# Optimization experiments

Measured on AMD Instinct MI355X. Metric: run time of the kernel, lower is better.

## Reference

```python
import jax, jax.numpy as jnp
import numpy as np

LN_EPS = 1e-5


def setup_inputs() -> dict:
    key = jax.random.key(0)
    ks = jax.random.split(key, 6)
    N_NODES, N_EDGES, D, H, E = 100000, 20000, 128, 64, 1000000
    node_feat = jax.random.normal(ks[0], (N_NODES, D), dtype=jnp.float32)
    edge_feat = jax.random.normal(ks[1], (N_EDGES, D), dtype=jnp.float32)
    gamma = jnp.ones((2 * D,), dtype=jnp.float32)
    beta = jnp.zeros((2 * D,), dtype=jnp.float32)
    # xavier_uniform-like init
    lim1 = float(np.sqrt(6.0 / (2 * D + H)))
    lim2 = float(np.sqrt(6.0 / (H + 1)))
    W1 = jax.random.uniform(ks[2], (2 * D, H), minval=-lim1, maxval=lim1, dtype=jnp.float32)
    b1 = jnp.zeros((H,), dtype=jnp.float32)
    W2 = jax.random.uniform(ks[3], (H, 1), minval=-lim2, maxval=lim2, dtype=jnp.float32)
    b2 = jnp.zeros((1,), dtype=jnp.float32)
    node_idx = jax.random.randint(ks[4], (E,), 0, N_NODES, dtype=jnp.int64 if jax.config.read('jax_enable_x64') else jnp.int32)
    edge_idx = jax.random.randint(ks[5], (E,), 0, N_EDGES, dtype=node_idx.dtype)
    return {"node_feat": node_feat, "edge_feat": edge_feat, "gamma": gamma, "beta": beta,
            "W1": W1, "b1": b1, "W2": W2, "b2": b2,
            "node_idx": node_idx, "edge_idx": edge_idx}


def reference(node_feat, edge_feat, gamma, beta, W1, b1, W2, b2, node_idx, edge_idx):
    # Gather incidence-pair embeddings: [E, D] each
    emb_node = node_feat[node_idx]
    emb_edge = edge_feat[edge_idx]
    # combined: [E, 2D], order = [edge, node] as in torch.cat([emb_edge, emb_node], 1)
    combined = jnp.concatenate([emb_edge, emb_node], axis=1)
    # LayerNorm over last dim
    mu = jnp.mean(combined, axis=-1, keepdims=True)
    var = jnp.var(combined, axis=-1, keepdims=True)
    xn = (combined - mu) * jax.lax.rsqrt(var + LN_EPS) * gamma + beta
    # MLP: Linear -> ReLU -> Linear, output [E, 1]
    h = jax.nn.relu(xn @ W1 + b1)
    return h @ W2 + b2
```

## Files before the change

### kernel.cpp

```cpp
#include <hip/hip_runtime.h>

#define LN_EPS 1e-5f
#define DD 128
#define TWO_D 256
#define HH 64
#define PPB 512

typedef unsigned int uint;
typedef unsigned short ushort;
typedef __attribute__((ext_vector_type(8))) short short8v;
typedef __attribute__((ext_vector_type(4))) float f32x4;

__device__ __forceinline__ ushort f2bf(float f) {
    uint u = __float_as_uint(f);
    u += 0x7FFFu + ((u >> 16) & 1u);
    return (ushort)(u >> 16);
}
__device__ __forceinline__ float bf2f(ushort h) {
    return __uint_as_float(((uint)h) << 16);
}
__device__ __forceinline__ int clampi(int v, int lo, int hi) {
    return v < lo ? lo : (v > hi ? hi : v);
}
__device__ __forceinline__ uint lsb8(uint a, uint b) {
    uint nx = (((a & 0x01010101u) * 0x08040201u) >> 24) & 0xFu;
    uint ny = (((b & 0x01010101u) * 0x08040201u) >> 24) & 0xFu;
    return (nx << 4) | ny;
}

__global__ __launch_bounds__(256) void k_fused(
    const float* __restrict__ node_feat, int n_nodes, int nbN,
    const float* __restrict__ edge_feat, int n_edges,
    const float* __restrict__ gamma, const float* __restrict__ beta,
    const float* __restrict__ W1, const float* __restrict__ b1,
    const float* __restrict__ W2,
    signed char* __restrict__ node_pt, signed char* __restrict__ edge_pt,
    float* __restrict__ GB) {
    int bid = blockIdx.x;
    int tid = threadIdx.x;

    if (bid == 0) {
        if (tid < 128) {
            int h = tid & 63;
            bool isB = tid >= 64;
            float acc = isB ? b1[h] : 0.f;
            const float* coef = isB ? beta : gamma;
#pragma unroll 8
            for (int d = 0; d < TWO_D; ++d)
                acc = fmaf(coef[d], W1[d * HH + h], acc);
            GB[tid] = acc;
        }
        __syncthreads();
        if (tid < 64) {
            int h = ((tid & 3) * 16) + (tid >> 2);
            GB[128 + tid] = GB[h];
            GB[192 + tid] = GB[64 + h];
            GB[256 + tid] = W2[h];
        }
        return;
    }

    const float* feat;
    int nrows, gofs, rbase0;
    signed char* pt;
    if (bid <= nbN) {
        feat = node_feat; nrows = n_nodes; gofs = 128;
        rbase0 = (bid - 1) * 128; pt = node_pt;
    } else {
        feat = edge_feat; nrows = n_edges; gofs = 0;
        rbase0 = (bid - 1 - nbN) * 128; pt = edge_pt;
    }

    __shared__ __align__(16) char lds[49664];
    uint* sqLDS = (uint*)(lds + 49152);

    {
        int l = tid & 63;
        int w = tid >> 6;
#pragma unroll
        for (int ci = 0; ci < 4; ++ci) {
            int combo = ci * 4 + w;
            int ks = combo & 3;
            int ht = combo >> 2;
            int kbase = gofs + ks * 32 + (l >> 4) * 8;
            int h = ht * 16 + (l & 15);
            short8v v;
#pragma unroll
            for (int j = 0; j < 8; ++j)
                v[j] = (short)f2bf(gamma[kbase + j] * W1[(size_t)(kbase + j) * HH + h]);
            *(short8v*)(lds + 32768 + combo * 1024 + l * 16) = v;
        }
    }

    {
        float4 tmp[16];
#pragma unroll
        for (int u = 0; u < 16; ++u) {
            int F4 = u * 256 + tid;
            int r = F4 >> 5;
            int rg = rbase0 + r;
            rg = rg < nrows ? rg : (nrows - 1);
            int c4 = (F4 & 31) * 4;
            tmp[u] = *(const float4*)&feat[(size_t)rg * DD + c4];
        }
#pragma unroll
        for (int u = 0; u < 16; ++u) {
            int F4 = u * 256 + tid;
            int r = F4 >> 5;
            int c4 = (F4 & 31) * 4;
            uint2 wv;
            wv.x = (uint)f2bf(tmp[u].x) | ((uint)f2bf(tmp[u].y) << 16);
            wv.y = (uint)f2bf(tmp[u].z) | ((uint)f2bf(tmp[u].w) << 16);
            int byte = (r * 256 + c4 * 2) ^ ((r & 7) << 4);
            *(uint2*)(lds + byte) = wv;
        }
    }

    __syncthreads();

    int w = tid >> 6;
    int lane = tid & 63;
    f32x4 acc[2][4];
#pragma unroll
    for (int i = 0; i < 2; ++i)
#pragma unroll
        for (int j = 0; j < 4; ++j) acc[i][j] = (f32x4){0.f, 0.f, 0.f, 0.f};

    int arow_lo = lane & 15;
    int akofs = (lane >> 4) * 8;
#pragma unroll
    for (int ks = 0; ks < 4; ++ks) {
        int kk = ks * 32 + akofs;
        int rr0 = (2 * w) * 16 + arow_lo;
        int rr1 = rr0 + 16;
        short8v a0 = *(const short8v*)(lds + ((rr0 * 256 + kk * 2) ^ ((rr0 & 7) << 4)));
        short8v a1 = *(const short8v*)(lds + ((rr1 * 256 + kk * 2) ^ ((rr1 & 7) << 4)));
#pragma unroll
        for (int ht = 0; ht < 4; ++ht) {
            short8v b = *(const short8v*)(lds + 32768 + (ht * 4 + ks) * 1024 + lane * 16);
            acc[0][ht] = __builtin_amdgcn_mfma_f32_16x16x32_bf16(a0, b, acc[0][ht], 0, 0, 0);
            acc[1][ht] = __builtin_amdgcn_mfma_f32_16x16x32_bf16(a1, b, acc[1][ht], 0, 0, 0);
        }
    }

    {
        int row = tid >> 1, half = tid & 1;
        float s = 0.f, q = 0.f;
#pragma unroll
        for (int i = 0; i < 8; ++i) {
            int byte = (row * 256 + half * 128 + i * 16) ^ ((row & 7) << 4);
            short8v v = *(const short8v*)(lds + byte);
#pragma unroll
            for (int j = 0; j < 8; ++j) {
                float x = bf2f((ushort)v[j]);
                s += x;
                q = fmaf(x, x, q);
            }
        }
        s += __shfl_xor(s, 1);
        q += __shfl_xor(q, 1);
        if (half == 0) {
            int sq = clampi(__float2int_rn(2.0f * s), -127, 127);
            int qq = clampi(__float2int_rn((q - 128.0f) * (1.0f / 0.75f)), -127, 127);
            sqLDS[row] = ((uint)sq & 0xFFu) | (((uint)qq & 0xFFu) << 8);
        }
    }

    __syncthreads();

    {
        int colh = lane & 15;
        int rquad = lane >> 4;
#pragma unroll
        for (int rt = 0; rt < 2; ++rt)
#pragma unroll
            for (int reg = 0; reg < 4; ++reg) {
                float m = fmaxf(fmaxf(fabsf(acc[rt][0][reg]), fabsf(acc[rt][1][reg])),
                                fmaxf(fabsf(acc[rt][2][reg]), fabsf(acc[rt][3][reg])));
                m = fmaxf(m, __shfl_xor(m, 1));
                m = fmaxf(m, __shfl_xor(m, 2));
                m = fmaxf(m, __shfl_xor(m, 4));
                m = fmaxf(m, __shfl_xor(m, 8));
                m = fmaxf(m, 1e-20f);
                float inv = 127.0f / m;
                int rl = (2 * w + rt) * 16 + rquad * 4 + reg;
                uint P = sqLDS[rl] | ((uint)f2bf(m * (1.0f / 127.0f)) << 16);
                uint pk = 0;
#pragma unroll
                for (int ht = 0; ht < 4; ++ht) {
                    uint byte;
                    if (colh < 8) {
                        int kpos = colh * 4 + ht;
                        uint V = (P >> (8 * (kpos >> 3))) & 0xFFu;
                        uint bit = (V >> (7 - (kpos & 7))) & 1u;
                        int q7 = clampi(__float2int_rn(acc[rt][ht][reg] * inv * 0.5f), -63, 63);
                        byte = (((uint)q7 << 1) | bit) & 0xFFu;
                    } else {
                        byte = (uint)__float2int_rn(acc[rt][ht][reg] * inv) & 0xFFu;
                    }
                    pk |= byte << (8 * ht);
                }
                if (rbase0 + rl < nrows)
                    *(uint*)&pt[(size_t)(rbase0 + rl) * 64 + colh * 4] = pk;
            }
    }
}

__global__ __launch_bounds__(256) void k_pairs(const int* __restrict__ node_idx,
                                               const int* __restrict__ edge_idx,
                                               const signed char* __restrict__ node_pt,
                                               const signed char* __restrict__ edge_pt,
                                               const float* __restrict__ GB,
                                               const float* __restrict__ b2,
                                               float* __restrict__ out, int E) {
    __shared__ int sNi[PPB];
    __shared__ int sEi[PPB];
    int tid = threadIdx.x;
    int base = blockIdx.x * PPB;
    int cnt = E - base;
    cnt = cnt < PPB ? cnt : PPB;
    for (int i = tid; i < cnt; i += 256) {
        sNi[i] = node_idx[base + i];
        sEi[i] = edge_idx[base + i];
    }
    __syncthreads();

    int l = tid & 3;
    int grp = tid >> 2;

    float G16[16], B16[16], W16[16];
#pragma unroll
    for (int j4 = 0; j4 < 4; ++j4) {
        float4 g = *(const float4*)&GB[128 + l * 16 + j4 * 4];
        float4 b = *(const float4*)&GB[192 + l * 16 + j4 * 4];
        float4 wv = *(const float4*)&GB[256 + l * 16 + j4 * 4];
        G16[j4 * 4 + 0] = g.x; G16[j4 * 4 + 1] = g.y; G16[j4 * 4 + 2] = g.z; G16[j4 * 4 + 3] = g.w;
        B16[j4 * 4 + 0] = b.x; B16[j4 * 4 + 1] = b.y; B16[j4 * 4 + 2] = b.z; B16[j4 * 4 + 3] = b.w;
        W16[j4 * 4 + 0] = wv.x; W16[j4 * 4 + 1] = wv.y; W16[j4 * 4 + 2] = wv.z; W16[j4 * 4 + 3] = wv.w;
    }
    float b2v = b2[0];
    int s_l = (l < 2) ? 1 : 0;
    float two_s = (l < 2) ? 2.0f : 1.0f;

    for (int it = 0; it < PPB; it += 256) {
        uint4 qe[4], qn[4];
        int iv[4];
#pragma unroll
        for (int u = 0; u < 4; ++u) {
            int i = it + u * 64 + grp;
            iv[u] = i;
            int ii = i < cnt ? i : 0;
            int ni = sNi[ii];
            int ei = sEi[ii];
            qe[u] = *(const uint4*)&edge_pt[(size_t)ei * 64 + l * 16];
            qn[u] = *(const uint4*)&node_pt[(size_t)ni * 64 + l * 16];
        }
#pragma unroll
        for (int u = 0; u < 4; ++u) {
            uint4 e = qe[u], n = qn[u];
            uint uu = lsb8(e.x, e.y) | (lsb8(e.z, e.w) << 8) |
                      (lsb8(n.x, n.y) << 16) | (lsb8(n.z, n.w) << 24);
            uint t0 = __shfl((int)uu, 0, 4);
            uint t1 = __shfl((int)uu, 1, 4);

            float S = 0.5f * ((float)(int)(signed char)(t0 & 0xFFu) +
                              (float)(int)(signed char)((t0 >> 16) & 0xFFu));
            float Q = 256.0f + 0.75f * ((float)(int)(signed char)((t0 >> 8) & 0xFFu) +
                                        (float)(int)(signed char)(t0 >> 24));
            float esc = bf2f((ushort)(t1 & 0xFFFFu)) * two_s;
            float nsc = bf2f((ushort)(t1 >> 16)) * two_s;

            float mu = S * (1.f / TWO_D);
            float var = fmaf(Q, 1.f / TWO_D, -mu * mu);
            float rstd = rsqrtf(var + LN_EPS);
            float nmu = -mu;

            uint ew[4] = {e.x, e.y, e.z, e.w};
            uint nw[4] = {n.x, n.y, n.z, n.w};
            float acc = 0.f;
#pragma unroll
            for (int j = 0; j < 16; ++j) {
                int sh = (3 - (j & 3)) * 8;
                int qa = ((int)(ew[j >> 2] << sh)) >> (24 + s_l);
                int qb = ((int)(nw[j >> 2] << sh)) >> (24 + s_l);
                float v = fmaf((float)qa, esc, (float)qb * nsc);
                float t = fmaf(nmu, G16[j], v);
                float hv = fmaf(rstd, t, B16[j]);
                hv = fmaxf(hv, 0.f);
                acc = fmaf(hv, W16[j], acc);
            }

            acc += __shfl_xor(acc, 1);
            acc += __shfl_xor(acc, 2);

            if (l == 0 && iv[u] < cnt) out[base + iv[u]] = acc + b2v;
        }
    }
}

extern "C" void kernel_launch(void* const* d_in, const int* in_sizes, int n_in,
                              void* d_out, int out_size, void* d_ws, size_t ws_size,
                              hipStream_t stream) {
    const float* node_feat = (const float*)d_in[0];
    const float* edge_feat = (const float*)d_in[1];
    const float* gamma = (const float*)d_in[2];
    const float* beta = (const float*)d_in[3];
    const float* W1 = (const float*)d_in[4];
    const float* b1 = (const float*)d_in[5];
    const float* W2 = (const float*)d_in[6];
    const float* b2 = (const float*)d_in[7];
    const int* node_idx = (const int*)d_in[8];
    const int* edge_idx = (const int*)d_in[9];

    int n_nodes = in_sizes[0] / DD;
    int n_edges = in_sizes[1] / DD;
    int E = in_sizes[8];

    char* wsb = (char*)d_ws;
    size_t o = 0;
    float* GB = (float*)(wsb + o); o += 2048;
    o = (o + 127) & ~(size_t)127;
    signed char* node_pt = (signed char*)(wsb + o); o += (size_t)n_nodes * 64;
    signed char* edge_pt = (signed char*)(wsb + o); o += (size_t)n_edges * 64;

    int nbN = (n_nodes + 127) / 128;
    int nbE = (n_edges + 127) / 128;

    k_fused<<<1 + nbN + nbE, 256, 0, stream>>>(node_feat, n_nodes, nbN,
                                               edge_feat, n_edges,
                                               gamma, beta, W1, b1, W2,
                                               node_pt, edge_pt, GB);
    k_pairs<<<(E + PPB - 1) / PPB, 256, 0, stream>>>(node_idx, edge_idx, node_pt, edge_pt,
                                                     GB, b2, (float*)d_out, E);
}
```

Measured before the change: 51.02 us.

## Bin incidence pairs by node index range before gathering packed rows

Adds histogram, scan and scatter kernels that sort the pairs into 8 buckets by node index range and pack node and edge indices into one record. A new pairs kernel walks each bucket so the concurrent node-row gathers hit a smaller slice of the packed node table, improving cache locality. The cost is three extra launches plus writing and reading an 8-byte-per-pair binned array, and output writes become scattered.

```diff
diff --git a/kernel.cpp b/kernel.cpp
--- a/kernel.cpp
+++ b/kernel.cpp
@@ -206,6 +206,181 @@
     }
 }
 
+__global__ __launch_bounds__(256) void k_hist(const int* __restrict__ node_idx, int E,
+                                              int chunk, float scale,
+                                              uint* __restrict__ hist) {
+    __shared__ uint lc[8];
+    int tid = threadIdx.x;
+    if (tid < 8) lc[tid] = 0;
+    __syncthreads();
+    int s = blockIdx.x * chunk;
+    int e = s + chunk < E ? s + chunk : E;
+    for (int p = s + tid; p < e; p += 256) {
+        int ni = __builtin_nontemporal_load(&node_idx[p]);
+        int b = (int)((float)ni * scale);
+        b = b < 7 ? b : 7;
+        atomicAdd(&lc[b], 1u);
+    }
+    __syncthreads();
+    if (tid < 8) hist[blockIdx.x * 8 + tid] = lc[tid];
+}
+
+__global__ __launch_bounds__(256) void k_scan(const uint* __restrict__ hist,
+                                              uint* __restrict__ offs,
+                                              uint* __restrict__ bstart, int E) {
+    __shared__ uint sc[256][8];
+    __shared__ uint bs_l[9];
+    int t = threadIdx.x;
+    uint orig[8];
+#pragma unroll
+    for (int b = 0; b < 8; ++b) {
+        orig[b] = hist[t * 8 + b];
+        sc[t][b] = orig[b];
+    }
+    __syncthreads();
+    for (int d = 1; d < 256; d <<= 1) {
+        uint v[8];
+        bool has = t >= d;
+        if (has) {
+#pragma unroll
+            for (int b = 0; b < 8; ++b) v[b] = sc[t - d][b];
+        }
+        __syncthreads();
+        if (has) {
+#pragma unroll
+            for (int b = 0; b < 8; ++b) sc[t][b] += v[b];
+        }
+        __syncthreads();
+    }
+    if (t == 0) {
+        uint bs = 0;
+#pragma unroll
+        for (int b = 0; b < 8; ++b) { bs_l[b] = bs; bs += sc[255][b]; }
+        bs_l[8] = bs;
+    }
+    __syncthreads();
+#pragma unroll
+    for (int b = 0; b < 8; ++b) offs[t * 8 + b] = bs_l[b] + sc[t][b] - orig[b];
+    if (t < 9) bstart[t] = bs_l[t];
+}
+
+__global__ __launch_bounds__(256) void k_scatter(const int* __restrict__ node_idx,
+                                                 const int* __restrict__ edge_idx,
+                                                 int E, int chunk, float scale,
+                                                 const uint* __restrict__ offs,
+                                                 uint2* __restrict__ binned) {
+    __shared__ uint lofs[8];
+    int tid = threadIdx.x;
+    if (tid < 8) lofs[tid] = offs[blockIdx.x * 8 + tid];
+    __syncthreads();
+    int s = blockIdx.x * chunk;
+    int e = s + chunk < E ? s + chunk : E;
+    for (int p = s + tid; p < e; p += 256) {
+        int ni = __builtin_nontemporal_load(&node_idx[p]);
+        int ei = __builtin_nontemporal_load(&edge_idx[p]);
+        int b = (int)((float)ni * scale);
+        b = b < 7 ? b : 7;
+        uint pos = atomicAdd(&lofs[b], 1u);
+        binned[pos] = make_uint2((uint)ni | ((uint)ei << 17), (uint)p);
+    }
+}
+
+__global__ __launch_bounds__(256) void k_pairs_b(const uint2* __restrict__ binned,
+                                                 const uint* __restrict__ bstart,
+                                                 const signed char* __restrict__ node_pt,
+                                                 const signed char* __restrict__ edge_pt,
+                                                 const float* __restrict__ GB,
+                                                 const float* __restrict__ b2,
+                                                 float* __restrict__ out) {
+    int bucket = blockIdx.x & 7;
+    uint nchunk = gridDim.x >> 3;
+    uint chunk = blockIdx.x >> 3;
+    uint s0 = bstart[bucket], s1 = bstart[bucket + 1];
+    uint sz = s1 - s0;
+    uint per = (sz + nchunk - 1) / nchunk;
+    uint beg = s0 + chunk * per;
+    if (beg >= s1) return;
+    uint end = beg + per;
+    end = end < s1 ? end : s1;
+
+    int tid = threadIdx.x;
+    int l = tid & 3;
+    int grp = tid >> 2;
+
+    float G16[16], B16[16], W16[16];
+#pragma unroll
+    for (int j4 = 0; j4 < 4; ++j4) {
+        float4 g = *(const float4*)&GB[128 + l * 16 + j4 * 4];
+        float4 b = *(const float4*)&GB[192 + l * 16 + j4 * 4];
+        float4 wv = *(const float4*)&GB[256 + l * 16 + j4 * 4];
+        G16[j4 * 4 + 0] = g.x; G16[j4 * 4 + 1] = g.y; G16[j4 * 4 + 2] = g.z; G16[j4 * 4 + 3] = g.w;
+        B16[j4 * 4 + 0] = b.x; B16[j4 * 4 + 1] = b.y; B16[j4 * 4 + 2] = b.z; B16[j4 * 4 + 3] = b.w;
+        W16[j4 * 4 + 0] = wv.x; W16[j4 * 4 + 1] = wv.y; W16[j4 * 4 + 2] = wv.z; W16[j4 * 4 + 3] = wv.w;
+    }
+    float b2v = b2[0];
+    int s_l = (l < 2) ? 1 : 0;
+    float two_s = (l < 2) ? 2.0f : 1.0f;
+
+    for (uint it = beg; it < end; it += 256) {
+        uint4 qe[4], qn[4];
+        uint pv[4];
+        bool valid[4];
+#pragma unroll
+        for (int u = 0; u < 4; ++u) {
+            uint i = it + (uint)u * 64 + (uint)grp;
+            bool v = i < end;
+            uint2 rec = binned[v ? i : beg];
+            uint ni = rec.x & 0x1FFFFu;
+            uint ei = rec.x >> 17;
+            qe[u] = *(const uint4*)&edge_pt[(size_t)ei * 64 + l * 16];
+            qn[u] = *(const uint4*)&node_pt[(size_t)ni * 64 + l * 16];
+            pv[u] = rec.y;
+            valid[u] = v;
+        }
+#pragma unroll
+        for (int u = 0; u < 4; ++u) {
+            uint4 e = qe[u], n = qn[u];
+            uint uu = lsb8(e.x, e.y) | (lsb8(e.z, e.w) << 8) |
+                      (lsb8(n.x, n.y) << 16) | (lsb8(n.z, n.w) << 24);
+            uint t0 = __shfl((int)uu, 0, 4);
+            uint t1 = __shfl((int)uu, 1, 4);
+
+            float S = 0.5f * ((float)(int)(signed char)(t0 & 0xFFu) +
+                              (float)(int)(signed char)((t0 >> 16) & 0xFFu));
+            float Q = 256.0f + 0.75f * ((float)(int)(signed char)((t0 >> 8) & 0xFFu) +
+                                        (float)(int)(signed char)(t0 >> 24));
+            float esc = bf2f((ushort)(t1 & 0xFFFFu)) * two_s;
+            float nsc = bf2f((ushort)(t1 >> 16)) * two_s;
+
+            float mu = S * (1.f / TWO_D);
+            float var = fmaf(Q, 1.f / TWO_D, -mu * mu);
+            float rstd = rsqrtf(var + LN_EPS);
+            float nmu = -mu;
+
+            uint ew[4] = {e.x, e.y, e.z, e.w};
+            uint nw[4] = {n.x, n.y, n.z, n.w};
+            float acc = 0.f;
+#pragma unroll
+            for (int j = 0; j < 16; ++j) {
+                int sh = (3 - (j & 3)) * 8;
+                int qa = ((int)(ew[j >> 2] << sh)) >> (24 + s_l);
+                int qb = ((int)(nw[j >> 2] << sh)) >> (24 + s_l);
+                float v = fmaf((float)qa, esc, (float)qb * nsc);
+                float t = fmaf(nmu, G16[j], v);
+                float hv = fmaf(rstd, t, B16[j]);
+                hv = fmaxf(hv, 0.f);
+                acc = fmaf(hv, W16[j], acc);
+            }
+
+            acc += __shfl_xor(acc, 1);
+            acc += __shfl_xor(acc, 2);
+
+            if (l == 0 && valid[u])
+                __builtin_nontemporal_store(acc + b2v, &out[pv[u]]);
+        }
+    }
+}
+
 __global__ __launch_bounds__(256) void k_pairs(const int* __restrict__ node_idx,
                                                const int* __restrict__ edge_idx,
                                                const signed char* __restrict__ node_pt,
@@ -319,17 +494,39 @@
     char* wsb = (char*)d_ws;
     size_t o = 0;
     float* GB = (float*)(wsb + o); o += 2048;
+    uint* hist = (uint*)(wsb + o); o += 256 * 8 * 4;
+    uint* offs = (uint*)(wsb + o); o += 256 * 8 * 4;
+    uint* bstart = (uint*)(wsb + o); o += 64;
     o = (o + 127) & ~(size_t)127;
     signed char* node_pt = (signed char*)(wsb + o); o += (size_t)n_nodes * 64;
     signed char* edge_pt = (signed char*)(wsb + o); o += (size_t)n_edges * 64;
+    o = (o + 127) & ~(size_t)127;
+    uint2* binned = (uint2*)(wsb + o);
+    size_t need = o + (size_t)E * sizeof(uint2);
+
+    bool can_bin = (n_nodes <= (1 << 17)) && (n_edges <= (1 << 15)) && (ws_size >= need);
 
     int nbN = (n_nodes + 127) / 128;
     int nbE = (n_edges + 127) / 128;
+    int chunk = (E + 255) / 256;
+    float scale = 8.0f / (float)n_nodes;
+
+    if (can_bin) {
+        k_hist<<<256, 256, 0, stream>>>(node_idx, E, chunk, scale, hist);
+        k_scan<<<1, 256, 0, stream>>>(hist, offs, bstart, E);
+        k_scatter<<<256, 256, 0, stream>>>(node_idx, edge_idx, E, chunk, scale, offs, binned);
+    }
 
     k_fused<<<1 + nbN + nbE, 256, 0, stream>>>(node_feat, n_nodes, nbN,
                                                edge_feat, n_edges,
                                                gamma, beta, W1, b1, W2,
                                                node_pt, edge_pt, GB);
-    k_pairs<<<(E + PPB - 1) / PPB, 256, 0, stream>>>(node_idx, edge_idx, node_pt, edge_pt,
-                                                     GB, b2, (float*)d_out, E);
-}
+
+    if (can_bin) {
+        k_pairs_b<<<2048, 256, 0, stream>>>(binned, bstart, node_pt, edge_pt,
+                                            GB, b2, (float*)d_out);
+    } else {
+        k_pairs<<<(E + PPB - 1) / PPB, 256, 0, stream>>>(node_idx, edge_idx, node_pt, edge_pt,
+                                                         GB, b2, (float*)d_out, E);
+    }
+}
```

After: 77.17 us. 1.51x slower.
